# Optimization experiments

Hardware: AMD Instinct MI355X
Metric: run time of the kernel (lower is better)

## Reference

```python
import jax, jax.numpy as jnp
import numpy as np

LOG8 = float(np.log(8.0))


def setup_inputs() -> dict:
    key = jax.random.key(0)
    ks = jax.random.split(key, 5)
    B, T, D = 4, 4096, 1024
    s = 1.0 / float(np.sqrt(D))  # torch default Linear init scale
    return {
        "x": jax.random.normal(ks[0], (B, T, D), dtype=jnp.float32),
        "h": jnp.zeros((B, D), dtype=jnp.float32),
        "W_r": jax.random.uniform(ks[1], (D, D), jnp.float32, -s, s),
        "b_r": jax.random.uniform(ks[2], (D,), jnp.float32, -4.0, -2.0),
        "W_i": jax.random.uniform(ks[3], (D, D), jnp.float32, -s, s),
        "b_i": jnp.zeros((D,), dtype=jnp.float32),
        "W_x": jax.random.uniform(ks[4], (D, D), jnp.float32, -s, s),
    }


def reference(x, h, W_r, b_r, W_i, b_i, W_x):
    # x: (B, T, D); torch Linear is y = x @ W.T + b with W of shape (out, in)
    r = jax.nn.sigmoid(jnp.einsum('btd,ed->bte', x, W_r) + b_r)   # recurrence gate
    i = jax.nn.sigmoid(jnp.einsum('btd,ed->bte', x, W_i) + b_i)   # input gate
    a = jnp.exp(-jax.nn.softplus(LOG8 * r))                        # data-dependent decay in (0,1)
    gate = jnp.sqrt(jnp.clip(1.0 - a * a, 1e-6))
    u = gate * (i * jnp.einsum('btd,ed->bte', x, W_x))             # per-step input term

    # diagonal linear recurrence h_t = a_t * h_{t-1} + u_t, scanned over time
    def step(h_prev, au):
        a_t, u_t = au  # each (B, D)
        h_new = a_t * h_prev + u_t
        return h_new, h_new

    a_t = jnp.swapaxes(a, 0, 1)  # (T, B, D)
    u_t = jnp.swapaxes(u, 0, 1)
    h_last, out = jax.lax.scan(step, h, (a_t, u_t))
    output = jnp.swapaxes(out, 0, 1)  # (B, T, D)
    return output, h_last
```

## Files before the change

### kernel.cpp

```cpp
#include <hip/hip_runtime.h>
#include <stdint.h>

#define D_DIM 1024
#define T_DIM 4096
#define B_DIM 4
#define M_DIM 16384
#define NX 16777216UL
#define NW 1048576UL
#define LOG8F 2.0794415416798357f
#define CHUNK_L 64
#define NCHUNK 64
#define WARM 16
#define NT 32

typedef __attribute__((ext_vector_type(4))) float f32x4;
typedef __attribute__((ext_vector_type(8))) short bf16x8;

__device__ __forceinline__ unsigned short f2bf(float f) {
    unsigned u = __float_as_uint(f);
    u += 0x7fffu + ((u >> 16) & 1u);
    return (unsigned short)(u >> 16);
}
__device__ __forceinline__ float unp_lo(unsigned p) { return __uint_as_float(p << 16); }
__device__ __forceinline__ float unp_hi(unsigned p) { return __uint_as_float(p & 0xffff0000u); }
__device__ __forceinline__ float sigm(float x) { return 1.0f / (1.0f + __expf(-x)); }

__device__ __forceinline__ void gl_lds16(const void* g, void* l) {
    __builtin_amdgcn_global_load_lds(
        (const __attribute__((address_space(1))) void*)g,
        (__attribute__((address_space(3))) void*)l, 16, 0, 0);
}

__global__ __launch_bounds__(256) void cvt_kernel(
    const float* __restrict__ x, const float* __restrict__ Wr,
    const float* __restrict__ Wi, const float* __restrict__ Wx,
    unsigned short* __restrict__ xb, unsigned short* __restrict__ wb)
{
    size_t tid = (size_t)blockIdx.x * 256 + threadIdx.x;
    size_t i = tid * 4;
    const float* src;
    unsigned short* dst;
    size_t off;
    if (i < NX) {
        src = x; dst = xb; off = i;
    } else {
        size_t j = i - NX;
        size_t w = j >> 20;
        off = j & (NW - 1);
        src = (w == 0) ? Wr : (w == 1 ? Wi : Wx);
        dst = wb + w * NW;
    }
    float4 v = *(const float4*)(src + off);
    ushort4 o;
    o.x = f2bf(v.x); o.y = f2bf(v.y); o.z = f2bf(v.z); o.w = f2bf(v.w);
    *(ushort4*)(dst + off) = o;
}

__global__ __launch_bounds__(512, 2) void fused_gemm(
    const unsigned short* __restrict__ xb, const unsigned short* __restrict__ wb,
    const float* __restrict__ b_r, const float* __restrict__ b_i,
    unsigned short* __restrict__ a_out, float* __restrict__ u_out)
{
    __shared__ __align__(16) unsigned short lds[4][4][4096];

    const int tid  = threadIdx.x;
    const int lane = tid & 63;
    const int wave = tid >> 6;
    const int wm = wave & 1;
    const int wn = wave >> 1;
    const int m0 = ((int)blockIdx.x >> 3) * 128;
    const int d0 = ((int)blockIdx.x & 7) * 128;
    const int frow = lane & 15;
    const int kgrp = lane >> 4;

    const int r0 = tid >> 2;
    const int cgs = (tid & 3) ^ ((r0 >> 1) & 3);
    const unsigned short* srcA = xb + (size_t)(m0 + r0) * D_DIM + cgs * 8;
    const unsigned short* srcB = wb + (size_t)(d0 + r0) * D_DIM + cgs * 8;

    int offA[4], offB[2];
    #pragma unroll
    for (int i = 0; i < 4; i++) {
        const int row = wm * 64 + i * 16 + frow;
        offA[i] = row * 32 + ((kgrp ^ ((row >> 1) & 3)) << 3);
    }
    #pragma unroll
    for (int j = 0; j < 2; j++) {
        const int row = wn * 32 + j * 16 + frow;
        offB[j] = row * 32 + ((kgrp ^ ((row >> 1) & 3)) << 3);
    }

    f32x4 acc[3][4][2];
    #pragma unroll
    for (int w = 0; w < 3; w++)
        #pragma unroll
        for (int i = 0; i < 4; i++)
            #pragma unroll
            for (int j = 0; j < 2; j++) acc[w][i][j] = (f32x4){0.f, 0.f, 0.f, 0.f};

    auto stage = [&](int t) {
        const int buf = t & 3;
        const int k0 = t << 5;
        gl_lds16(srcA + k0, &lds[buf][0][tid * 8]);
        #pragma unroll
        for (int w = 0; w < 3; w++)
            gl_lds16(srcB + (size_t)w * NW + k0, &lds[buf][1 + w][tid * 8]);
    };

    stage(0); stage(1); stage(2);

#define TILE_BODY(T, VM)                                                      \
    {                                                                         \
        asm volatile("s_waitcnt vmcnt(" #VM ")" ::: "memory");                \
        __builtin_amdgcn_s_barrier();                                         \
        if ((T) + 3 < NT) stage((T) + 3);                                     \
        const int buf = (T) & 3;                                              \
        bf16x8 af[4], bfr[3][2];                                              \
        _Pragma("unroll")                                                     \
        for (int i = 0; i < 4; i++)                                           \
            af[i] = *(const bf16x8*)&lds[buf][0][offA[i]];                    \
        _Pragma("unroll")                                                     \
        for (int w = 0; w < 3; w++)                                           \
            _Pragma("unroll")                                                 \
            for (int j = 0; j < 2; j++)                                       \
                bfr[w][j] = *(const bf16x8*)&lds[buf][1 + w][offB[j]];        \
        __builtin_amdgcn_s_setprio(1);                                        \
        _Pragma("unroll")                                                     \
        for (int w = 0; w < 3; w++)                                           \
            _Pragma("unroll")                                                 \
            for (int i = 0; i < 4; i++)                                       \
                _Pragma("unroll")                                             \
                for (int j = 0; j < 2; j++)                                   \
                    acc[w][i][j] = __builtin_amdgcn_mfma_f32_16x16x32_bf16(   \
                        af[i], bfr[w][j], acc[w][i][j], 0, 0, 0);             \
        __builtin_amdgcn_s_setprio(0);                                        \
    }

    for (int t = 0; t < NT - 3; ++t) TILE_BODY(t, 8);
    TILE_BODY(NT - 3, 8);
    TILE_BODY(NT - 2, 4);
    TILE_BODY(NT - 1, 0);
#undef TILE_BODY

    const int mb = m0 + wm * 64 + kgrp * 4;
    const int db = d0 + wn * 32 + frow;
    #pragma unroll
    for (int j = 0; j < 2; j++) {
        const int d = db + j * 16;
        const float br = b_r[d];
        const float bi = b_i[d];
        #pragma unroll
        for (int i = 0; i < 4; i++) {
            const int m = mb + i * 16;
            #pragma unroll
            for (int r = 0; r < 4; r++) {
                const size_t idx = (size_t)(m + r) * D_DIM + d;
                float rg = sigm(acc[0][i][j][r] + br);
                float a = sigm(-LOG8F * rg);
                a_out[idx] = f2bf(a);
                float g = sqrtf(fmaxf(1.0f - a * a, 1e-6f));
                u_out[idx] = g * sigm(acc[1][i][j][r] + bi) * acc[2][i][j][r];
            }
        }
    }
}

__global__ __launch_bounds__(256) void scan_warm(
    const unsigned short* __restrict__ a, const float* __restrict__ u,
    const float* __restrict__ h0, float* __restrict__ hstart)
{
    int tid = blockIdx.x * 256 + threadIdx.x;
    int d = (tid & 511) << 1;
    int bc = tid >> 9;
    int b = bc >> 6;
    int c = bc & (NCHUNK - 1);
    float hx, hy;
    if (c == 0) {
        float2 h = *(const float2*)(h0 + b * D_DIM + d);
        hx = h.x; hy = h.y;
    } else {
        hx = 0.0f; hy = 0.0f;
        size_t base = ((size_t)b * T_DIM + (size_t)c * CHUNK_L - WARM) * D_DIM + d;
        #pragma unroll 4
        for (int t = 0; t < WARM; t++) {
            size_t idx = base + (size_t)t * D_DIM;
            unsigned ap = *(const unsigned*)(a + idx);
            float2 uv = *(const float2*)(u + idx);
            hx = unp_lo(ap) * hx + uv.x;
            hy = unp_hi(ap) * hy + uv.y;
        }
    }
    *(float2*)(hstart + bc * D_DIM + d) = make_float2(hx, hy);
}

__global__ __launch_bounds__(256) void scan_apply(
    const unsigned short* __restrict__ a, const float* __restrict__ hstart,
    float* __restrict__ out)
{
    int tid = blockIdx.x * 256 + threadIdx.x;
    int d = (tid & 511) << 1;
    int bc = tid >> 9;
    int b = bc >> 6;
    int c = bc & (NCHUNK - 1);
    size_t base = ((size_t)b * T_DIM + (size_t)c * CHUNK_L) * D_DIM + d;
    float2 h = *(const float2*)(hstart + bc * D_DIM + d);
    float hx = h.x, hy = h.y;
    #pragma unroll 4
    for (int t = 0; t < CHUNK_L; t++) {
        size_t idx = base + (size_t)t * D_DIM;
        unsigned ap = *(const unsigned*)(a + idx);
        float2 uv = *(const float2*)(out + idx);
        hx = unp_lo(ap) * hx + uv.x;
        hy = unp_hi(ap) * hy + uv.y;
        *(float2*)(out + idx) = make_float2(hx, hy);
    }
    if (c == NCHUNK - 1)
        *(float2*)(out + (size_t)M_DIM * D_DIM + b * D_DIM + d) = make_float2(hx, hy);
}

extern "C" void kernel_launch(void* const* d_in, const int* in_sizes, int n_in,
                              void* d_out, int out_size, void* d_ws, size_t ws_size,
                              hipStream_t stream)
{
    const float* x  = (const float*)d_in[0];
    const float* h0 = (const float*)d_in[1];
    const float* Wr = (const float*)d_in[2];
    const float* br = (const float*)d_in[3];
    const float* Wi = (const float*)d_in[4];
    const float* bi = (const float*)d_in[5];
    const float* Wx = (const float*)d_in[6];
    float* out = (float*)d_out;

    char* ws = (char*)d_ws;
    unsigned short* xb = (unsigned short*)ws;
    unsigned short* wb = (unsigned short*)(ws + 33554432);
    unsigned short* a_buf = (unsigned short*)(ws + 33554432 + 6291456);
    float* hstart = (float*)(ws + 33554432 + 6291456 + 33554432);

    cvt_kernel<<<19456, 256, 0, stream>>>(x, Wr, Wi, Wx, xb, wb);
    fused_gemm<<<1024, 512, 0, stream>>>(xb, wb, br, bi, a_buf, out);
    scan_warm<<<512, 256, 0, stream>>>(a_buf, out, h0, hstart);
    scan_apply<<<512, 256, 0, stream>>>(a_buf, hstart, out);
}
```

Before: 286.6 us.

## Enlarge GEMM M-tile to 256 rows and use triple-buffered LDS pipeline

Each fused GEMM block now computes 256 rows of x against 128 output columns for all three weight matrices, doubling the accumulators per wave to 48 MFMA tiles. This halves the grid and improves reuse of each loaded weight tile. The LDS ring drops from four stages to three to fit the larger A tile, and the inner loop now loads one A fragment at a time. The cost is higher register pressure (192 accumulator VGPRs), the loss of the two-blocks-per-CU launch bound, and a shallower prefetch depth.

```diff
diff --git a/kernel.cpp b/kernel.cpp
--- a/kernel.cpp
+++ b/kernel.cpp
@@ -56,93 +56,95 @@
     *(ushort4*)(dst + off) = o;
 }
 
-__global__ __launch_bounds__(512, 2) void fused_gemm(
+__global__ __launch_bounds__(512) void fused_gemm(
     const unsigned short* __restrict__ xb, const unsigned short* __restrict__ wb,
     const float* __restrict__ b_r, const float* __restrict__ b_i,
     unsigned short* __restrict__ a_out, float* __restrict__ u_out)
 {
-    __shared__ __align__(16) unsigned short lds[4][4][4096];
+    __shared__ __align__(16) unsigned short lds[3][20480];
 
     const int tid  = threadIdx.x;
     const int lane = tid & 63;
     const int wave = tid >> 6;
     const int wm = wave & 1;
     const int wn = wave >> 1;
-    const int m0 = ((int)blockIdx.x >> 3) * 128;
+    const int m0 = ((int)blockIdx.x >> 3) * 256;
     const int d0 = ((int)blockIdx.x & 7) * 128;
     const int frow = lane & 15;
     const int kgrp = lane >> 4;
 
     const int r0 = tid >> 2;
     const int cgs = (tid & 3) ^ ((r0 >> 1) & 3);
-    const unsigned short* srcA = xb + (size_t)(m0 + r0) * D_DIM + cgs * 8;
-    const unsigned short* srcB = wb + (size_t)(d0 + r0) * D_DIM + cgs * 8;
-
-    int offA[4], offB[2];
-    #pragma unroll
-    for (int i = 0; i < 4; i++) {
-        const int row = wm * 64 + i * 16 + frow;
+    const unsigned short* srcA  = xb + (size_t)(m0 + r0) * D_DIM + cgs * 8;
+    const unsigned short* srcB0 = wb + (size_t)(d0 + r0) * D_DIM + cgs * 8;
+    const unsigned short* srcB1 = srcB0 + NW;
+    const unsigned short* srcB2 = srcB0 + 2 * NW;
+
+    int offA[8], offB[3][2];
+    #pragma unroll
+    for (int i = 0; i < 8; i++) {
+        const int row = wm * 128 + i * 16 + frow;
         offA[i] = row * 32 + ((kgrp ^ ((row >> 1) & 3)) << 3);
     }
-    #pragma unroll
-    for (int j = 0; j < 2; j++) {
-        const int row = wn * 32 + j * 16 + frow;
-        offB[j] = row * 32 + ((kgrp ^ ((row >> 1) & 3)) << 3);
-    }
-
-    f32x4 acc[3][4][2];
     #pragma unroll
     for (int w = 0; w < 3; w++)
         #pragma unroll
-        for (int i = 0; i < 4; i++)
+        for (int j = 0; j < 2; j++) {
+            const int row = wn * 32 + j * 16 + frow;
+            offB[w][j] = 8192 + w * 4096 + row * 32 + ((kgrp ^ ((row >> 1) & 3)) << 3);
+        }
+
+    f32x4 acc[3][8][2];
+    #pragma unroll
+    for (int w = 0; w < 3; w++)
+        #pragma unroll
+        for (int i = 0; i < 8; i++)
             #pragma unroll
             for (int j = 0; j < 2; j++) acc[w][i][j] = (f32x4){0.f, 0.f, 0.f, 0.f};
 
     auto stage = [&](int t) {
-        const int buf = t & 3;
+        const int buf = t % 3;
         const int k0 = t << 5;
-        gl_lds16(srcA + k0, &lds[buf][0][tid * 8]);
-        #pragma unroll
-        for (int w = 0; w < 3; w++)
-            gl_lds16(srcB + (size_t)w * NW + k0, &lds[buf][1 + w][tid * 8]);
+        gl_lds16(srcA  + k0,          &lds[buf][tid * 8]);
+        gl_lds16(srcA  + 131072 + k0, &lds[buf][(tid + 512) * 8]);
+        gl_lds16(srcB0 + k0,          &lds[buf][8192 + tid * 8]);
+        gl_lds16(srcB1 + k0,          &lds[buf][12288 + tid * 8]);
+        gl_lds16(srcB2 + k0,          &lds[buf][16384 + tid * 8]);
     };
 
-    stage(0); stage(1); stage(2);
+    stage(0); stage(1);
 
 #define TILE_BODY(T, VM)                                                      \
     {                                                                         \
         asm volatile("s_waitcnt vmcnt(" #VM ")" ::: "memory");                \
         __builtin_amdgcn_s_barrier();                                         \
-        if ((T) + 3 < NT) stage((T) + 3);                                     \
-        const int buf = (T) & 3;                                              \
-        bf16x8 af[4], bfr[3][2];                                              \
-        _Pragma("unroll")                                                     \
-        for (int i = 0; i < 4; i++)                                           \
-            af[i] = *(const bf16x8*)&lds[buf][0][offA[i]];                    \
+        if ((T) + 2 < NT) stage((T) + 2);                                     \
+        const int buf = (T) % 3;                                              \
+        bf16x8 bfr[3][2];                                                     \
         _Pragma("unroll")                                                     \
         for (int w = 0; w < 3; w++)                                           \
             _Pragma("unroll")                                                 \
             for (int j = 0; j < 2; j++)                                       \
-                bfr[w][j] = *(const bf16x8*)&lds[buf][1 + w][offB[j]];        \
-        __builtin_amdgcn_s_setprio(1);                                        \
+                bfr[w][j] = *(const bf16x8*)&lds[buf][offB[w][j]];            \
         _Pragma("unroll")                                                     \
-        for (int w = 0; w < 3; w++)                                           \
+        for (int i = 0; i < 8; i++) {                                         \
+            bf16x8 af = *(const bf16x8*)&lds[buf][offA[i]];                   \
+            __builtin_amdgcn_s_setprio(1);                                    \
             _Pragma("unroll")                                                 \
-            for (int i = 0; i < 4; i++)                                       \
+            for (int w = 0; w < 3; w++)                                       \
                 _Pragma("unroll")                                             \
                 for (int j = 0; j < 2; j++)                                   \
                     acc[w][i][j] = __builtin_amdgcn_mfma_f32_16x16x32_bf16(   \
-                        af[i], bfr[w][j], acc[w][i][j], 0, 0, 0);             \
-        __builtin_amdgcn_s_setprio(0);                                        \
-    }
-
-    for (int t = 0; t < NT - 3; ++t) TILE_BODY(t, 8);
-    TILE_BODY(NT - 3, 8);
-    TILE_BODY(NT - 2, 4);
+                        af, bfr[w][j], acc[w][i][j], 0, 0, 0);                \
+            __builtin_amdgcn_s_setprio(0);                                    \
+        }                                                                     \
+    }
+
+    for (int t = 0; t < NT - 1; ++t) TILE_BODY(t, 5);
     TILE_BODY(NT - 1, 0);
 #undef TILE_BODY
 
-    const int mb = m0 + wm * 64 + kgrp * 4;
+    const int mb = m0 + wm * 128 + kgrp * 4;
     const int db = d0 + wn * 32 + frow;
     #pragma unroll
     for (int j = 0; j < 2; j++) {
@@ -150,7 +152,7 @@
         const float br = b_r[d];
         const float bi = b_i[d];
         #pragma unroll
-        for (int i = 0; i < 4; i++) {
+        for (int i = 0; i < 8; i++) {
             const int m = mb + i * 16;
             #pragma unroll
             for (int r = 0; r < 4; r++) {
@@ -238,7 +240,7 @@
     float* hstart = (float*)(ws + 33554432 + 6291456 + 33554432);
 
     cvt_kernel<<<19456, 256, 0, stream>>>(x, Wr, Wi, Wx, xb, wb);
-    fused_gemm<<<1024, 512, 0, stream>>>(xb, wb, br, bi, a_buf, out);
+    fused_gemm<<<512, 512, 0, stream>>>(xb, wb, br, bi, a_buf, out);
     scan_warm<<<512, 256, 0, stream>>>(a_buf, out, h0, hstart);
     scan_apply<<<512, 256, 0, stream>>>(a_buf, hstart, out);
 }
```

Measured after the change: 282.9 us. No clear change (-1.3%).

## Double-buffer LDS fragment reads in registers to overlap with MFMA

Applied to the files above, without the earlier changes.

Restructures the GEMM main loop so that the LDS fragments for tile t+1 are read into a second register set while the MFMAs for tile t run, ping-ponging between two register buffers. Shared memory is flattened to one dimension with precomputed offsets for each weight, and the vmcnt waits are adjusted so the next tile's data is resident one step earlier. The aim is to hide LDS read latency behind matrix math. In exchange it roughly doubles the fragment register footprint, which may hurt occupancy under launch_bounds(512,2), and the waits and barriers are more delicate to get right.

```diff
diff --git a/kernel.cpp b/kernel.cpp
--- a/kernel.cpp
+++ b/kernel.cpp
@@ -61,7 +61,7 @@
     const float* __restrict__ b_r, const float* __restrict__ b_i,
     unsigned short* __restrict__ a_out, float* __restrict__ u_out)
 {
-    __shared__ __align__(16) unsigned short lds[4][4][4096];
+    __shared__ __align__(16) unsigned short lds[4][16384];
 
     const int tid  = threadIdx.x;
     const int lane = tid & 63;
@@ -75,20 +75,24 @@
 
     const int r0 = tid >> 2;
     const int cgs = (tid & 3) ^ ((r0 >> 1) & 3);
-    const unsigned short* srcA = xb + (size_t)(m0 + r0) * D_DIM + cgs * 8;
-    const unsigned short* srcB = wb + (size_t)(d0 + r0) * D_DIM + cgs * 8;
-
-    int offA[4], offB[2];
+    const unsigned short* srcA  = xb + (size_t)(m0 + r0) * D_DIM + cgs * 8;
+    const unsigned short* srcB0 = wb + (size_t)(d0 + r0) * D_DIM + cgs * 8;
+    const unsigned short* srcB1 = srcB0 + NW;
+    const unsigned short* srcB2 = srcB0 + 2 * NW;
+
+    int offA[4], offB[3][2];
     #pragma unroll
     for (int i = 0; i < 4; i++) {
         const int row = wm * 64 + i * 16 + frow;
         offA[i] = row * 32 + ((kgrp ^ ((row >> 1) & 3)) << 3);
     }
     #pragma unroll
-    for (int j = 0; j < 2; j++) {
-        const int row = wn * 32 + j * 16 + frow;
-        offB[j] = row * 32 + ((kgrp ^ ((row >> 1) & 3)) << 3);
-    }
+    for (int w = 0; w < 3; w++)
+        #pragma unroll
+        for (int j = 0; j < 2; j++) {
+            const int row = wn * 32 + j * 16 + frow;
+            offB[w][j] = (1 + w) * 4096 + row * 32 + ((kgrp ^ ((row >> 1) & 3)) << 3);
+        }
 
     f32x4 acc[3][4][2];
     #pragma unroll
@@ -101,29 +105,42 @@
     auto stage = [&](int t) {
         const int buf = t & 3;
         const int k0 = t << 5;
-        gl_lds16(srcA + k0, &lds[buf][0][tid * 8]);
-        #pragma unroll
-        for (int w = 0; w < 3; w++)
-            gl_lds16(srcB + (size_t)w * NW + k0, &lds[buf][1 + w][tid * 8]);
+        gl_lds16(srcA  + k0, &lds[buf][tid * 8]);
+        gl_lds16(srcB0 + k0, &lds[buf][4096 + tid * 8]);
+        gl_lds16(srcB1 + k0, &lds[buf][8192 + tid * 8]);
+        gl_lds16(srcB2 + k0, &lds[buf][12288 + tid * 8]);
     };
 
+    bf16x8 af_a[4], af_b[4], bf_a[3][2], bf_b[3][2];
+
     stage(0); stage(1); stage(2);
-
-#define TILE_BODY(T, VM)                                                      \
+    asm volatile("s_waitcnt vmcnt(8)" ::: "memory");
+    __builtin_amdgcn_s_barrier();
+    asm volatile("" ::: "memory");
+    #pragma unroll
+    for (int i = 0; i < 4; i++) af_a[i] = *(const bf16x8*)&lds[0][offA[i]];
+    #pragma unroll
+    for (int w = 0; w < 3; w++)
+        #pragma unroll
+        for (int j = 0; j < 2; j++) bf_a[w][j] = *(const bf16x8*)&lds[0][offB[w][j]];
+
+#define STEP(T, AFC, BFC, AFN, BFN, VM)                                       \
     {                                                                         \
         asm volatile("s_waitcnt vmcnt(" #VM ")" ::: "memory");                \
         __builtin_amdgcn_s_barrier();                                         \
+        asm volatile("" ::: "memory");                                        \
         if ((T) + 3 < NT) stage((T) + 3);                                     \
-        const int buf = (T) & 3;                                              \
-        bf16x8 af[4], bfr[3][2];                                              \
-        _Pragma("unroll")                                                     \
-        for (int i = 0; i < 4; i++)                                           \
-            af[i] = *(const bf16x8*)&lds[buf][0][offA[i]];                    \
-        _Pragma("unroll")                                                     \
-        for (int w = 0; w < 3; w++)                                           \
+        if ((T) + 1 < NT) {                                                   \
+            const unsigned short* nb = lds[((T) + 1) & 3];                    \
             _Pragma("unroll")                                                 \
-            for (int j = 0; j < 2; j++)                                       \
-                bfr[w][j] = *(const bf16x8*)&lds[buf][1 + w][offB[j]];        \
+            for (int i = 0; i < 4; i++)                                       \
+                AFN[i] = *(const bf16x8*)&nb[offA[i]];                        \
+            _Pragma("unroll")                                                 \
+            for (int w = 0; w < 3; w++)                                       \
+                _Pragma("unroll")                                             \
+                for (int j = 0; j < 2; j++)                                   \
+                    BFN[w][j] = *(const bf16x8*)&nb[offB[w][j]];              \
+        }                                                                     \
         __builtin_amdgcn_s_setprio(1);                                        \
         _Pragma("unroll")                                                     \
         for (int w = 0; w < 3; w++)                                           \
@@ -132,15 +149,19 @@
                 _Pragma("unroll")                                             \
                 for (int j = 0; j < 2; j++)                                   \
                     acc[w][i][j] = __builtin_amdgcn_mfma_f32_16x16x32_bf16(   \
-                        af[i], bfr[w][j], acc[w][i][j], 0, 0, 0);             \
+                        AFC[i], BFC[w][j], acc[w][i][j], 0, 0, 0);            \
         __builtin_amdgcn_s_setprio(0);                                        \
     }
 
-    for (int t = 0; t < NT - 3; ++t) TILE_BODY(t, 8);
-    TILE_BODY(NT - 3, 8);
-    TILE_BODY(NT - 2, 4);
-    TILE_BODY(NT - 1, 0);
-#undef TILE_BODY
+    for (int t = 0; t < 28; t += 2) {
+        STEP(t,     af_a, bf_a, af_b, bf_b, 4);
+        STEP(t + 1, af_b, bf_b, af_a, bf_a, 4);
+    }
+    STEP(28, af_a, bf_a, af_b, bf_b, 4);
+    STEP(29, af_b, bf_b, af_a, bf_a, 4);
+    STEP(30, af_a, bf_a, af_b, bf_b, 0);
+    STEP(31, af_b, bf_b, af_a, bf_a, 0);
+#undef STEP
 
     const int mb = m0 + wm * 64 + kgrp * 4;
     const int db = d0 + wn * 32 + frow;
```

Measured after the change: 288.4 us. About the same (+0.6%).
